# Kernel optimization log

Measured on AMD Instinct MI355X. Metric: run time of the kernel, lower is better.

Reference implementation:

```python
import jax, jax.numpy as jnp
import numpy as np

B, T, D = 1, 1024, 1024
H = 16; HKV = 16; HD = D // H; R = 2; K = 3; LOWR = 32
HR = HKV * R                      # heads after harmonic expansion
OUTW = HKV * HD * 2 * R           # w_proj output width
SCALE = HD ** -0.5


def setup_inputs() -> dict:
    key = jax.random.key(0)
    ks = jax.random.split(key, 10)
    def rn(k, shape, sc=1.0):
        return jax.random.normal(k, shape, dtype=jnp.float32) * sc
    return {
        'hidden_states': rn(ks[0], (B, T, D)),
        'q_w': rn(ks[1], (D, D), D ** -0.5),
        'k_w': rn(ks[2], (D, D), D ** -0.5),
        'v_w': rn(ks[3], (D, D), D ** -0.5),
        'w1': rn(ks[4], (LOWR, D), D ** -0.5),
        'w2': rn(ks[5], (OUTW, LOWR), LOWR ** -0.5),
        'conv_w': rn(ks[6], (OUTW, K), K ** -0.5),
        'bt_w': rn(ks[7], (HKV * R, D), D ** -0.5),
        'bt_b': jnp.zeros((HKV * R,), jnp.float32),
        'o_w': rn(ks[8], (D, D * R), (D * R) ** -0.5),
        'omega': 0.01 * jnp.ones((1, 1, 1, R), jnp.float32),
        'phi': jnp.zeros((1, 1, 1, R), jnp.float32),
    }


def path_attention_forward(hidden_states, q_w, k_w, v_w, w1, w2, conv_w,
                           bt_w, bt_b, o_w, omega, phi):
    b, t, _ = hidden_states.shape
    q = hidden_states @ q_w.T
    k = hidden_states @ k_w.T
    v = hidden_states @ v_w.T
    # low-rank w projection, causal depthwise short conv (kernel K), SiLU
    w_raw = (hidden_states @ w1.T) @ w2.T                    # [b,t,OUTW]
    xp = jnp.pad(w_raw, ((0, 0), (K - 1, 0), (0, 0)))
    w_raw = sum(xp[:, i:i + t, :] * conv_w[:, i] for i in range(K))
    w_raw = jax.nn.silu(w_raw)
    # rotary-like harmonic mixing of Householder directions
    w5 = w_raw.reshape(b, t, HKV, 2 * R, HD)
    Ah = w5[:, :, :, 0::2, :]                                # [b,t,HKV,R,HD]
    Bh = w5[:, :, :, 1::2, :]
    pos = jnp.arange(t, dtype=jnp.float32)[None, :, None, None]
    theta = omega * pos + phi                                # [1,t,1,R]
    c = jnp.cos(theta)[..., None]
    s = jnp.sin(theta)[..., None]
    Wdir = Ah * c + Bh * s
    Wdir = Wdir * jax.lax.rsqrt(jnp.sum(Wdir * Wdir, -1, keepdims=True) + 1e-6)
    beta = jax.nn.sigmoid(hidden_states @ bt_w.T + bt_b) * 2.0   # [b,t,HR]
    # repeat-interleave q/k/v heads across harmonics -> [b,HR,t,HD]
    to_h = lambda x: jnp.swapaxes(jnp.repeat(x.reshape(b, t, H, HD), R, axis=2), 1, 2)
    qh, kh, vh = to_h(q), to_h(k), to_h(v)
    wh = jnp.swapaxes(Wdir.reshape(b, t, HR, HD), 1, 2)      # [b,HR,t,HD]
    bh = jnp.swapaxes(beta, 1, 2)                            # [b,HR,t]
    # PaTH logits: A_ij = q_i^T (H_i ... H_{j+1}) k_j, H_t = I - beta_t w_t w_t^T.
    # WY/UT transform: with M_ts = beta_t (w_t.w_s) for s<t, the coefficients
    # B_tj (t>j) of the accumulated rank-1 corrections solve the unit-lower
    # triangular system (I + M) B = strilow(Db W K^T), and
    # A = tril(Q K^T - tril(Q W^T) B).
    idx = jnp.arange(t)
    strict = idx[:, None] > idx[None, :]
    incl = idx[:, None] >= idx[None, :]
    Mw = jnp.where(strict, jnp.einsum('bhtd,bhsd->bhts', wh, wh) * bh[..., None], 0.0)
    rhs = jnp.where(strict, jnp.einsum('bhtd,bhjd->bhtj', wh, kh) * bh[..., None], 0.0)
    Bmat = jax.scipy.linalg.solve_triangular(Mw + jnp.eye(t, dtype=Mw.dtype), rhs, lower=True)
    qk = jnp.einsum('bhid,bhjd->bhij', qh, kh)
    qw = jnp.where(incl, jnp.einsum('bhid,bhtd->bhit', qh, wh), 0.0)
    logits = (qk - jnp.einsum('bhit,bhtj->bhij', qw, Bmat)) * SCALE
    logits = jnp.where(incl, logits, -1e30)
    p = jax.nn.softmax(logits, axis=-1)
    o = jnp.einsum('bhij,bhjd->bhid', p, vh)                 # [b,HR,t,HD]
    o = jnp.swapaxes(o, 1, 2).reshape(b, t, HR * HD)         # [b,t,D*R]
    return o @ o_w.T


def reference(hidden_states, q_w, k_w, v_w, w1, w2, conv_w, bt_w, bt_b, o_w, omega, phi):
    return path_attention_forward(hidden_states, q_w, k_w, v_w, w1, w2, conv_w,
                                  bt_w, bt_b, o_w, omega, phi)
```

## Files before the change

### kernel.cpp

```cpp
#include <hip/hip_runtime.h>
#include <math.h>

#define TTD 1024
#define DDM 1024
#define HDIM 64
#define PSC2 0.18033688011112042f
#define LS 72

typedef __attribute__((ext_vector_type(8))) __bf16 bf16x8;
typedef __attribute__((ext_vector_type(4))) float f32x4;
#define MFMA16(a,b,c) __builtin_amdgcn_mfma_f32_16x16x32_bf16(a,b,c,0,0,0)

#define STR_(x) #x
#define WAITVM(N) asm volatile("s_waitcnt vmcnt(" STR_(N) ")" ::: "memory")
#define BAR() do { __builtin_amdgcn_s_barrier(); asm volatile("" ::: "memory"); } while (0)
#define LGKBAR() do { asm volatile("s_waitcnt lgkmcnt(0)" ::: "memory"); \
                      __builtin_amdgcn_s_barrier(); asm volatile("" ::: "memory"); } while (0)
#define FULLBAR() do { asm volatile("s_waitcnt vmcnt(0) lgkmcnt(0)" ::: "memory"); \
                       __builtin_amdgcn_s_barrier(); asm volatile("" ::: "memory"); } while (0)

__device__ __forceinline__ ushort f2b(float f) {
  unsigned u = __builtin_bit_cast(unsigned, f);
  return (ushort)((u + 0x7fffu + ((u >> 16) & 1u)) >> 16);
}
__device__ __forceinline__ float b2f(ushort u) {
  unsigned v = (unsigned)u << 16;
  return __builtin_bit_cast(float, v);
}

__device__ __forceinline__ void gload_lds16(const ushort* g, ushort* l) {
  __builtin_amdgcn_global_load_lds(
      (const __attribute__((address_space(1))) unsigned*)g,
      (__attribute__((address_space(3))) unsigned*)l, 16, 0, 0);
}

#define SWZ(row, cc) (((row) * 8 + ((cc) ^ ((row) & 7))) * 8)
#define SWZE(row, col) (SWZ(row, (col) >> 3) + ((col) & 7))
#define SWZ2(row, cc) (((row) * 8 + ((cc) ^ (((row) & 7) ^ ((row) >> 3)))) * 8)
#define SWZ2E(row, col) (SWZ2(row, (col) >> 3) + ((col) & 7))

__device__ __forceinline__ void stage_tile(const ushort* gb, long gs, ushort* tile,
                                           int w, int l) {
  int sub = l >> 3, cc = (l & 7) ^ sub;
  #pragma unroll
  for (int it = 0; it < 2; ++it) {
    int q = w * 2 + it;
    gload_lds16(gb + (long)(q * 8 + sub) * gs + cc * 8, &tile[(q * 64 + l) * 8]);
  }
}

__device__ __forceinline__ bf16x8 frag(const ushort* tile, int row, int cc) {
  return *(const bf16x8*)&tile[SWZ(row, cc)];
}
__device__ __forceinline__ bf16x8 frag2(const ushort* tile, int row, int cc) {
  return *(const bf16x8*)&tile[SWZ2(row, cc)];
}

#define XT_PERH   557056L
#define OFF_X     0L
#define OFF_PZ    35651584L
#define OFF_HSB   35651584L
#define OFF_QWW   37748736L
#define OFF_KWW   39845888L
#define OFF_VWW   41943040L
#define OFF_W2B   44040192L
#define OFF_WLOWB 44302336L
#define OFF_TB    98566144L
#define OFF_OALL  98566144L
#define OFF_YB    102760448L
#define OFF_OWB   106954752L
#define OFF_WHB   111149056L
#define OFF_QB    115343360L
#define OFF_KB    117440512L
#define OFF_VTB   119537664L
#define OFF_BETA  121634816L
#define OFF_BW64  121765888L

#define CVT_TOTAL 6488064L
struct CvtSegs {
  const float* src[8];
  ushort* dst[8];
  long cnt[8];
};
__global__ __launch_bounds__(256) void cvt_all_kernel(CvtSegs sg) {
  long e = ((long)blockIdx.x * 256 + threadIdx.x) * 4;
  #pragma unroll
  for (int s = 0; s < 8; ++s) {
    if (e < sg.cnt[s]) {
      float4 f = *(const float4*)(sg.src[s] + e);
      ushort4 o;
      o.x = f2b(f.x); o.y = f2b(f.y); o.z = f2b(f.z); o.w = f2b(f.w);
      *(ushort4*)(sg.dst[s] + e) = o;
      return;
    }
    e -= sg.cnt[s];
  }
}

__global__ __launch_bounds__(256) void qkv_sp_kernel(
    const ushort* __restrict__ hsb,
    const ushort* __restrict__ wq, const ushort* __restrict__ wk, const ushort* __restrict__ wv,
    const ushort* __restrict__ bw, const float* __restrict__ bt_b,
    ushort* __restrict__ cq, ushort* __restrict__ ck, ushort* __restrict__ cv,
    float* __restrict__ beta, ushort* __restrict__ wlowb)
{
  int z = blockIdx.z;
  if (z == 3 && blockIdx.x != 0) return;
  const ushort* B = (z == 0) ? wq : (z == 1) ? wk : (z == 2) ? wv : bw;

  __shared__ ushort Ab[2][8192];
  __shared__ ushort Bb[2][4096];

  int tid = threadIdx.x, w = tid >> 6, l = tid & 63;
  int quad = l >> 4, lane15 = l & 15;
  int rm = blockIdx.y * 128, cn = (z == 3) ? 0 : blockIdx.x * 64;
  const ushort* Ag = hsb + (long)rm * DDM;
  const ushort* Bg = B + (long)cn * DDM;

  stage_tile(Ag, DDM, &Ab[0][0], w, l);
  stage_tile(Ag + 64 * DDM, DDM, &Ab[0][4096], w, l);
  stage_tile(Bg, DDM, &Bb[0][0], w, l);

  f32x4 acc[2][4] = {};
  int arow0 = (w & 1) * 32 + lane15;
  int asel = (w >> 1) * 4096;
  for (int kt = 0; kt < 16; ++kt) {
    int cur = kt & 1;
    if (kt < 15) {
      int nxt = cur ^ 1;
      stage_tile(Ag + (kt + 1) * 64, DDM, &Ab[nxt][0], w, l);
      stage_tile(Ag + 64 * DDM + (kt + 1) * 64, DDM, &Ab[nxt][4096], w, l);
      stage_tile(Bg + (kt + 1) * 64, DDM, &Bb[nxt][0], w, l);
      WAITVM(6);
    } else {
      WAITVM(0);
    }
    BAR();
    const ushort* Atile = &Ab[cur][asel];
    #pragma unroll
    for (int s = 0; s < 2; ++s) {
      bf16x8 a0 = frag(Atile, arow0, s * 4 + quad);
      bf16x8 a1 = frag(Atile, arow0 + 16, s * 4 + quad);
      #pragma unroll
      for (int f = 0; f < 4; ++f) {
        bf16x8 bf = frag(&Bb[cur][0], f * 16 + lane15, s * 4 + quad);
        acc[0][f] = MFMA16(a0, bf, acc[0][f]);
        acc[1][f] = MFMA16(a1, bf, acc[1][f]);
      }
    }
    BAR();
  }

  if (z < 2) {
    ushort* Cb = (z == 0) ? cq : ck;
    #pragma unroll
    for (int rr = 0; rr < 2; ++rr) {
      int orow = rm + w * 32 + rr * 16 + quad * 4;
      #pragma unroll
      for (int f = 0; f < 4; ++f)
        #pragma unroll
        for (int r = 0; r < 4; ++r)
          Cb[(long)(orow + r) * DDM + cn + f * 16 + lane15] = f2b(acc[rr][f][r]);
    }
  } else if (z == 2) {
    #pragma unroll
    for (int rr = 0; rr < 2; ++rr) {
      int orow = rm + w * 32 + rr * 16 + quad * 4;
      #pragma unroll
      for (int f = 0; f < 4; ++f) {
        ushort4 o;
        o.x = f2b(acc[rr][f][0]); o.y = f2b(acc[rr][f][1]);
        o.z = f2b(acc[rr][f][2]); o.w = f2b(acc[rr][f][3]);
        *(ushort4*)&cv[(long)(cn + f * 16 + lane15) * TTD + orow] = o;
      }
    }
  } else {
    #pragma unroll
    for (int rr = 0; rr < 2; ++rr) {
      int orow = rm + w * 32 + rr * 16 + quad * 4;
      #pragma unroll
      for (int f = 0; f < 2; ++f) {
        int hr = f * 16 + lane15;
        float bb = bt_b[hr];
        #pragma unroll
        for (int r = 0; r < 4; ++r)
          beta[(long)hr * TTD + orow + r] = 2.f / (1.f + __expf(-(acc[rr][f][r] + bb)));
      }
      #pragma unroll
      for (int f = 2; f < 4; ++f)
        #pragma unroll
        for (int r = 0; r < 4; ++r)
          wlowb[(long)(orow + r) * 32 + (f - 2) * 16 + lane15] = f2b(acc[rr][f][r]);
    }
  }
}

__global__ __launch_bounds__(256) void wraw_solveA_kernel(
    const ushort* __restrict__ wlowb, const ushort* __restrict__ w2b,
    const float* __restrict__ conv_w, const float* __restrict__ omega,
    const float* __restrict__ phi, const float* __restrict__ beta,
    ushort* __restrict__ whb, ushort* __restrict__ TB, ushort* __restrict__ YB)
{
  int c = blockIdx.x;
  int rm = c * 64;
  int p = blockIdx.y;
  int hkv = p >> 1, r = p & 1;
  int c0 = hkv * 256 + r * 128;

  __shared__ char pool_[65568];
  ushort* As = (ushort*)pool_;
  ushort* Bs = (ushort*)(pool_ + 4096);
  float (*WR)[132] = (float(*)[132])(pool_ + 12288);
  ushort* Wrow = (ushort*)(pool_ + 47136);
  ushort* WT   = (ushort*)(pool_ + 56352);
  float (*Lm)[65] = (float(*)[65])pool_;
  float (*Vf)[65] = (float(*)[65])(pool_ + 16640);
  ushort* Tb = (ushort*)(pool_ + 33280);

  int tid = threadIdx.x, w = tid >> 6, l = tid & 63;
  int quad = l >> 4, lane15 = l & 15;

  {
    int row = tid >> 2, ch = (tid & 3) * 8;
    gload_lds16(wlowb + (long)(rm + row) * 32 + ch, &As[row * 32 + ch]);
    gload_lds16(w2b + (long)(c0 + row) * 32 + ch, &Bs[row * 32 + ch]);
    gload_lds16(w2b + (long)(c0 + 64 + row) * 32 + ch, &Bs[(64 + row) * 32 + ch]);
  }
  {
    int hr2 = tid >> 7, col = tid & 127;
    float acc = 0.f;
    if (rm > 0) {
      long t = rm - 2 + hr2;
      for (int k = 0; k < 32; ++k)
        acc += b2f(wlowb[t * 32 + k]) * b2f(w2b[(long)(c0 + col) * 32 + k]);
    }
    WR[hr2][col] = acc;
  }
  FULLBAR();

  #pragma unroll
  for (int g = 0; g < 2; ++g) {
    f32x4 acc[4] = {};
    bf16x8 af = *(const bf16x8*)&As[(w * 16 + lane15) * 32 + quad * 8];
    #pragma unroll
    for (int f = 0; f < 4; ++f) {
      bf16x8 bf = *(const bf16x8*)&Bs[(g * 64 + f * 16 + lane15) * 32 + quad * 8];
      acc[f] = MFMA16(af, bf, acc[f]);
    }
    #pragma unroll
    for (int f = 0; f < 4; ++f)
      #pragma unroll
      for (int rr = 0; rr < 4; ++rr)
        WR[2 + w * 16 + quad * 4 + rr][g * 64 + f * 16 + lane15] = acc[f][rr];
  }
  LGKBAR();

  {
    float cwa[3], cwb[3];
    #pragma unroll
    for (int i = 0; i < 3; ++i) {
      cwa[i] = conv_w[(long)(c0 + l) * 3 + i];
      cwb[i] = conv_w[(long)(c0 + 64 + l) * 3 + i];
    }
    float om = omega[r], ph = phi[r];
    for (int it = 0; it < 16; ++it) {
      int tl = it * 4 + w;
      int t = rm + tl;
      float a = cwa[0] * WR[tl][l] + cwa[1] * WR[tl + 1][l] + cwa[2] * WR[tl + 2][l];
      float b = cwb[0] * WR[tl][64 + l] + cwb[1] * WR[tl + 1][64 + l] + cwb[2] * WR[tl + 2][64 + l];
      a = a / (1.f + __expf(-a));
      b = b / (1.f + __expf(-b));
      float th = om * (float)t + ph;
      float wd = a * __cosf(th) + b * __sinf(th);
      float ss = wd * wd;
      #pragma unroll
      for (int o = 32; o > 0; o >>= 1) ss += __shfl_xor(ss, o, 64);
      ushort hv = f2b(wd * (1.f / sqrtf(ss + 1e-6f)));
      whb[((long)p * TTD + t) * HDIM + l] = hv;
      Wrow[tl * LS + l] = hv;
      WT[l * LS + tl] = hv;
    }
  }
  LGKBAR();

  const float* bet = beta + (long)p * TTD + rm;
  ushort* TBh = TB + ((long)p * 16 + c) * 4096;
  ushort* YBh = YB + ((long)p * 16 + c) * 4096;

  f32x4 g4[4] = {};
  #pragma unroll
  for (int s = 0; s < 2; ++s) {
    bf16x8 af = *(const bf16x8*)&Wrow[(w * 16 + lane15) * LS + s * 32 + quad * 8];
    #pragma unroll
    for (int f = 0; f < 4; ++f) {
      bf16x8 bf = *(const bf16x8*)&Wrow[(f * 16 + lane15) * LS + s * 32 + quad * 8];
      g4[f] = MFMA16(af, bf, g4[f]);
    }
  }
  #pragma unroll
  for (int r4 = 0; r4 < 4; ++r4) {
    int t = w * 16 + quad * 4 + r4;
    float bv = bet[t];
    #pragma unroll
    for (int f = 0; f < 4; ++f) {
      int tp = f * 16 + lane15;
      Lm[t][tp] = (t > tp) ? bv * g4[f][r4] : 0.f;
    }
  }
  LGKBAR();

  {
    float cur[16];
    #pragma unroll
    for (int i = 0; i < 16; ++i) cur[i] = (w * 16 + i == l) ? bet[l] : 0.f;
    for (int sb = 0; sb < 4; ++sb) {
      if (w == sb) {
        float xloc[16];
        #pragma unroll
        for (int i = 0; i < 16; ++i) {
          float bv = cur[i];
          #pragma unroll
          for (int j2 = 0; j2 < 16; ++j2)
            if (j2 < i) bv -= Lm[sb * 16 + i][sb * 16 + j2] * xloc[j2];
          xloc[i] = bv;
          Vf[sb * 16 + i][l] = bv;
        }
      }
      LGKBAR();
      if (w > sb) {
        float xp[16];
        #pragma unroll
        for (int t = 0; t < 16; ++t) xp[t] = Vf[sb * 16 + t][l];
        #pragma unroll
        for (int i = 0; i < 16; ++i) {
          float s2 = cur[i];
          #pragma unroll
          for (int t = 0; t < 16; ++t) s2 -= Lm[w * 16 + i][sb * 16 + t] * xp[t];
          cur[i] = s2;
        }
      }
    }
  }
  {
    int t = tid >> 2, off = (tid & 3) * 16;
    ushort tmp[16];
    #pragma unroll
    for (int i = 0; i < 16; ++i) { tmp[i] = f2b(Vf[t][off + i]); Tb[t * LS + off + i] = tmp[i]; }
    *(uint4*)&TBh[t * 64 + off] = *(const uint4*)&tmp[0];
    *(uint4*)&TBh[t * 64 + off + 8] = *(const uint4*)&tmp[8];
  }
  LGKBAR();
  f32x4 y[4] = {};
  #pragma unroll
  for (int s = 0; s < 2; ++s) {
    bf16x8 af = *(const bf16x8*)&Tb[(w * 16 + lane15) * LS + s * 32 + quad * 8];
    #pragma unroll
    for (int f = 0; f < 4; ++f) {
      bf16x8 bf = *(const bf16x8*)&WT[(f * 16 + lane15) * LS + s * 32 + quad * 8];
      y[f] = MFMA16(af, bf, y[f]);
    }
  }
  #pragma unroll
  for (int f = 0; f < 4; ++f)
    #pragma unroll
    for (int r4 = 0; r4 < 4; ++r4)
      YBh[(long)(w * 16 + quad * 4 + r4) * 64 + f * 16 + lane15] = f2b(y[f][r4]);
}

__global__ __launch_bounds__(256) void solveB_kernel(
    const ushort* __restrict__ whb, const ushort* __restrict__ kb,
    const ushort* __restrict__ TB, const ushort* __restrict__ YB,
    ushort* __restrict__ Xb, ushort* __restrict__ KZ)
{
  int h = blockIdx.x;
  int ty = blockIdx.y;
  int js = (ty < 8) ? ty : (23 - ty);
  int j0 = js * 64;
  const ushort* wh_h = whb + (long)h * TTD * HDIM;
  const ushort* k_h = kb + (long)(h >> 1) * 64;
  ushort* X_h = Xb + (long)h * XT_PERH;
  ushort* KZ_h = KZ + (long)h * 15 * TTD * HDIM;
  int xidx = js * 16 - js * (js - 1) / 2;

  __shared__ ushort KT[4096];
  __shared__ ushort WT[4096];
  __shared__ ushort XM[4096];
  __shared__ ushort nS[4096];

  int tid = threadIdx.x, w = tid >> 6, l = tid & 63;
  int quad = l >> 4, lane15 = l & 15;
  f32x4 Sacc[4] = {}, Wacc[4] = {};

  stage_tile(k_h + (long)j0 * DDM, DDM, KT, w, l);

  float kreg[4][4];
  #pragma unroll
  for (int f = 0; f < 4; ++f)
    #pragma unroll
    for (int r = 0; r < 4; ++r)
      kreg[f][r] = b2f(k_h[(long)(j0 + w * 16 + quad * 4 + r) * DDM + f * 16 + lane15]);

  int prow0 = tid >> 3, pd0 = (tid & 7) * 8;
  uint4 pk0 = *(const uint4*)&wh_h[((long)js * 64 + prow0) * HDIM + pd0];
  uint4 pk1 = *(const uint4*)&wh_h[((long)js * 64 + 32 + prow0) * HDIM + pd0];
  bf16x8 ybr0 = {}, ybr1 = {};

  WAITVM(0);

  for (int c = js; c < 16; ++c) {
    LGKBAR();
    {
      const ushort* pu0 = (const ushort*)&pk0;
      const ushort* pu1 = (const ushort*)&pk1;
      #pragma unroll
      for (int i = 0; i < 8; ++i) WT[SWZ2E(pd0 + i, prow0)] = pu0[i];
      #pragma unroll
      for (int i = 0; i < 8; ++i) WT[SWZ2E(pd0 + i, 32 + prow0)] = pu1[i];
    }
    if (c < 15) {
      pk0 = *(const uint4*)&wh_h[((long)(c + 1) * 64 + prow0) * HDIM + pd0];
      pk1 = *(const uint4*)&wh_h[((long)(c + 1) * 64 + 32 + prow0) * HDIM + pd0];
    }
    f32x4 xacc[4] = {};
    if (c == js) {
      const ushort* whc = wh_h + (long)c * 64 * HDIM;
      f32x4 m[4] = {};
      #pragma unroll
      for (int s = 0; s < 2; ++s) {
        bf16x8 af = *(const bf16x8*)&whc[(long)(w * 16 + lane15) * HDIM + s * 32 + quad * 8];
        #pragma unroll
        for (int f = 0; f < 4; ++f)
          m[f] = MFMA16(af, frag(KT, f * 16 + lane15, s * 4 + quad), m[f]);
      }
      #pragma unroll
      for (int f = 0; f < 4; ++f)
        #pragma unroll
        for (int r = 0; r < 4; ++r) {
          int t = w * 16 + quad * 4 + r, j = f * 16 + lane15;
          XM[SWZE(j, t)] = (t > j) ? f2b(m[f][r]) : (ushort)0;
        }
      LGKBAR();
      const ushort* TBh = TB + ((long)h * 16 + c) * 4096;
      #pragma unroll
      for (int s = 0; s < 2; ++s) {
        bf16x8 af = *(const bf16x8*)&TBh[(long)(w * 16 + lane15) * 64 + s * 32 + quad * 8];
        #pragma unroll
        for (int f = 0; f < 4; ++f)
          xacc[f] = MFMA16(af, frag(XM, f * 16 + lane15, s * 4 + quad), xacc[f]);
      }
      LGKBAR();
    } else {
      #pragma unroll
      for (int f = 0; f < 4; ++f) {
        xacc[f] = MFMA16(ybr0, frag(KT, f * 16 + lane15, 0 * 4 + quad), xacc[f]);
        xacc[f] = MFMA16(ybr0, frag(nS, f * 16 + lane15, 0 * 4 + quad), xacc[f]);
        xacc[f] = MFMA16(ybr1, frag(KT, f * 16 + lane15, 1 * 4 + quad), xacc[f]);
        xacc[f] = MFMA16(ybr1, frag(nS, f * 16 + lane15, 1 * 4 + quad), xacc[f]);
      }
    }
    #pragma unroll
    for (int f = 0; f < 4; ++f)
      #pragma unroll
      for (int r = 0; r < 4; ++r)
        XM[SWZE(f * 16 + lane15, w * 16 + quad * 4 + r)] = f2b(xacc[f][r]);
    LGKBAR();
    {
      ushort* xt = X_h + (long)xidx * 4096;
      int j = tid >> 2, c2 = (tid & 3) * 2;
      bf16x8 s0 = frag(XM, j, c2);
      bf16x8 s1 = frag(XM, j, c2 + 1);
      *(bf16x8*)&xt[j * 64 + c2 * 8] = s0;
      *(bf16x8*)&xt[j * 64 + c2 * 8 + 8] = s1;
    }
    ++xidx;
    if (c < 15) {
      {
        const ushort* YBn = YB + ((long)h * 16 + c + 1) * 4096;
        ybr0 = *(const bf16x8*)&YBn[(long)(w * 16 + lane15) * 64 + 0 * 32 + quad * 8];
        ybr1 = *(const bf16x8*)&YBn[(long)(w * 16 + lane15) * 64 + 1 * 32 + quad * 8];
      }
      #pragma unroll
      for (int s = 0; s < 2; ++s) {
        bf16x8 aw = frag2(WT, w * 16 + lane15, s * 4 + quad);
        bf16x8 ax = frag(XM, w * 16 + lane15, s * 4 + quad);
        #pragma unroll
        for (int f = 0; f < 4; ++f) {
          Sacc[f] = MFMA16(aw, frag(XM, f * 16 + lane15, s * 4 + quad), Sacc[f]);
          Wacc[f] = MFMA16(ax, frag2(WT, f * 16 + lane15, s * 4 + quad), Wacc[f]);
        }
      }
      ushort* pz = KZ_h + (long)c * TTD * HDIM;
      #pragma unroll
      for (int f = 0; f < 4; ++f)
        #pragma unroll
        for (int r = 0; r < 4; ++r)
          pz[(long)(j0 + w * 16 + quad * 4 + r) * 64 + f * 16 + lane15] =
              f2b(kreg[f][r] - Wacc[f][r]);
      #pragma unroll
      for (int f = 0; f < 4; ++f)
        #pragma unroll
        for (int r = 0; r < 4; ++r)
          nS[SWZE(f * 16 + lane15, w * 16 + quad * 4 + r)] = f2b(-Sacc[f][r]);
    }
  }
}

__global__ __launch_bounds__(256) void flash_kernel(
    const ushort* __restrict__ qb, const ushort* __restrict__ kbuf,
    const ushort* __restrict__ whb, const ushort* __restrict__ Xb,
    const ushort* __restrict__ KZ, const ushort* __restrict__ vTb,
    ushort* __restrict__ oall)
{
  int h = blockIdx.x;
  int y = blockIdx.y;
  int ri = (y < 8) ? y : (23 - y);
  int r0 = ri * 64;
  const ushort* q_h = qb + (long)(h >> 1) * 64;
  const ushort* k_h = kbuf + (long)(h >> 1) * 64;
  const ushort* wh_h = whb + (long)h * TTD * HDIM;
  const ushort* X_h = Xb + (long)h * XT_PERH;
  const ushort* kz = KZ + ((long)h * 15 + (ri - 1)) * TTD * HDIM;
  const ushort* v_h = vTb + (long)(h >> 1) * 64 * TTD;

  __shared__ ushort S[2][3][4096];
  __shared__ ushort KD[4096];
  __shared__ ushort QWD[4096];
  __shared__ ushort PT[4096];

  int tid = threadIdx.x, w = tid >> 6, l = tid & 63;
  int quad = l >> 4, lane15 = l & 15;

  bf16x8 aq[2];
  #pragma unroll
  for (int s = 0; s < 2; ++s)
    aq[s] = *(const bf16x8*)&q_h[(long)(r0 + w * 16 + lane15) * DDM + s * 32 + quad * 8];
  bf16x8 kones;
  #pragma unroll
  for (int i = 0; i < 8; ++i) kones[i] = (__bf16)1.0f;
  const ushort* xst = X_h + (long)ri * 4096;
  stage_tile(k_h + (long)r0 * DDM, DDM, KD, w, l);
  if (ri > 0) stage_tile(kz, 64, &S[0][0][0], w, l);
  stage_tile(xst, 64, &S[0][1][0], w, l);
  stage_tile(v_h, TTD, &S[0][2][0], w, l);
  {
    f32x4 t4[4] = {};
    #pragma unroll
    for (int s = 0; s < 2; ++s)
      #pragma unroll
      for (int f = 0; f < 4; ++f) {
        bf16x8 bf = *(const bf16x8*)&wh_h[(long)(r0 + f * 16 + lane15) * HDIM + s * 32 + quad * 8];
        t4[f] = MFMA16(aq[s], bf, t4[f]);
      }
    #pragma unroll
    for (int f = 0; f < 4; ++f)
      #pragma unroll
      for (int r = 0; r < 4; ++r) {
        int i = w * 16 + quad * 4 + r, t = f * 16 + lane15;
        QWD[SWZE(i, t)] = (i >= t) ? f2b(-t4[f][r]) : (ushort)0;
      }
  }

  f32x4 O[4] = {};
  f32x4 O5 = {};
  float m[4];
  #pragma unroll
  for (int r = 0; r < 4; ++r) m[r] = -1e30f;

  for (int jb = 0; jb <= ri; ++jb) {
    int cur = jb & 1;
    const ushort* xnx = xst + (long)(15 - jb) * 4096;
    if (jb < ri) {
      long c0n = (long)(jb + 1) * 64;
      ushort* nb = &S[cur ^ 1][0][0];
      if (jb + 1 < ri) {
        stage_tile(kz + c0n * 64, 64, nb, w, l);
        stage_tile(xnx, 64, nb + 4096, w, l);
        stage_tile(v_h + c0n, TTD, nb + 8192, w, l);
        WAITVM(6);
      } else {
        stage_tile(xnx, 64, nb + 4096, w, l);
        stage_tile(v_h + c0n, TTD, nb + 8192, w, l);
        WAITVM(4);
      }
    } else {
      WAITVM(0);
    }
    BAR();
    const ushort* Skz = &S[cur][0][0];
    const ushort* Sx  = &S[cur][1][0];
    const ushort* Sv  = &S[cur][2][0];
    f32x4 acc[4] = {};
    const ushort* Sb = (jb < ri) ? Skz : KD;
    #pragma unroll
    for (int s = 0; s < 2; ++s)
      #pragma unroll
      for (int f = 0; f < 4; ++f)
        acc[f] = MFMA16(aq[s], frag(Sb, f * 16 + lane15, s * 4 + quad), acc[f]);
    #pragma unroll
    for (int s = 0; s < 2; ++s) {
      bf16x8 aw = frag(QWD, w * 16 + lane15, s * 4 + quad);
      #pragma unroll
      for (int f = 0; f < 4; ++f)
        acc[f] = MFMA16(aw, frag(Sx, f * 16 + lane15, s * 4 + quad), acc[f]);
    }
    float rmax[4] = {-3e38f, -3e38f, -3e38f, -3e38f};
    #pragma unroll
    for (int f = 0; f < 4; ++f)
      #pragma unroll
      for (int r = 0; r < 4; ++r) {
        float lv = acc[f][r] * PSC2;
        if (jb == ri && (f * 16 + lane15) > (w * 16 + quad * 4 + r)) lv = -3e38f;
        acc[f][r] = lv;
        rmax[r] = fmaxf(rmax[r], lv);
      }
    #pragma unroll
    for (int r = 0; r < 4; ++r) {
      rmax[r] = fmaxf(rmax[r], __shfl_xor(rmax[r], 1, 64));
      rmax[r] = fmaxf(rmax[r], __shfl_xor(rmax[r], 2, 64));
      rmax[r] = fmaxf(rmax[r], __shfl_xor(rmax[r], 4, 64));
      rmax[r] = fmaxf(rmax[r], __shfl_xor(rmax[r], 8, 64));
    }
    bool grow = (rmax[0] > m[0]) | (rmax[1] > m[1]) | (rmax[2] > m[2]) | (rmax[3] > m[3]);
    if (__any(grow)) {
      float alpha[4];
      #pragma unroll
      for (int r = 0; r < 4; ++r) {
        float nm = fmaxf(m[r], rmax[r]);
        alpha[r] = exp2f(m[r] - nm);
        m[r] = nm;
        O5[r] *= alpha[r];
      }
      #pragma unroll
      for (int f = 0; f < 4; ++f)
        #pragma unroll
        for (int r = 0; r < 4; ++r) O[f][r] *= alpha[r];
    }
    #pragma unroll
    for (int f = 0; f < 4; ++f)
      #pragma unroll
      for (int r = 0; r < 4; ++r)
        acc[f][r] = exp2f(acc[f][r] - m[r]);
    #pragma unroll
    for (int f = 0; f < 4; ++f)
      #pragma unroll
      for (int r = 0; r < 4; ++r) {
        int i = w * 16 + quad * 4 + r;
        PT[SWZE(i, f * 16 + lane15)] = f2b(acc[f][r]);
      }
    #pragma unroll
    for (int s = 0; s < 2; ++s) {
      bf16x8 ap = frag(PT, w * 16 + lane15, s * 4 + quad);
      #pragma unroll
      for (int f = 0; f < 4; ++f)
        O[f] = MFMA16(ap, frag(Sv, f * 16 + lane15, s * 4 + quad), O[f]);
      O5 = MFMA16(ap, kones, O5);
    }
    BAR();
    xst = xnx;
  }
  float lsum[4];
  #pragma unroll
  for (int r = 0; r < 4; ++r) lsum[r] = 1.f / O5[r];
  #pragma unroll
  for (int f = 0; f < 4; ++f)
    #pragma unroll
    for (int r = 0; r < 4; ++r)
      oall[(long)(r0 + w * 16 + quad * 4 + r) * 2048 + h * 64 + f * 16 + lane15] =
          f2b(O[f][r] * lsum[r]);
}

__global__ __launch_bounds__(256) void gemm_out_kernel(
    const ushort* __restrict__ A, const ushort* __restrict__ Bb, float* __restrict__ C)
{
  __shared__ ushort Ab[2][8192];
  __shared__ ushort Bt[2][8192];
  int tid = threadIdx.x, w = tid >> 6, l = tid & 63;
  int quad = l >> 4, lane15 = l & 15;
  int rm = blockIdx.y * 64, cn = blockIdx.x * 64;
  const ushort* Ag = A + (long)rm * 2048;
  const ushort* Bg = Bb + (long)cn * 2048;

  stage_tile(Ag, 2048, &Ab[0][0], w, l);
  stage_tile(Ag + 64, 2048, &Ab[0][4096], w, l);
  stage_tile(Bg, 2048, &Bt[0][0], w, l);
  stage_tile(Bg + 64, 2048, &Bt[0][4096], w, l);

  f32x4 acc[4] = {};
  for (int kt = 0; kt < 16; ++kt) {
    int cur = kt & 1;
    if (kt < 15) {
      int nxt = cur ^ 1;
      long o = (long)(kt + 1) * 128;
      stage_tile(Ag + o, 2048, &Ab[nxt][0], w, l);
      stage_tile(Ag + o + 64, 2048, &Ab[nxt][4096], w, l);
      stage_tile(Bg + o, 2048, &Bt[nxt][0], w, l);
      stage_tile(Bg + o + 64, 2048, &Bt[nxt][4096], w, l);
      WAITVM(8);
    } else {
      WAITVM(0);
    }
    BAR();
    #pragma unroll
    for (int u = 0; u < 2; ++u)
      #pragma unroll
      for (int s = 0; s < 2; ++s) {
        bf16x8 af = frag(&Ab[cur][u * 4096], w * 16 + lane15, s * 4 + quad);
        #pragma unroll
        for (int f = 0; f < 4; ++f)
          acc[f] = MFMA16(af, frag(&Bt[cur][u * 4096], f * 16 + lane15, s * 4 + quad), acc[f]);
      }
    BAR();
  }
  int orow = rm + w * 16 + quad * 4;
  #pragma unroll
  for (int f = 0; f < 4; ++f)
    #pragma unroll
    for (int r = 0; r < 4; ++r)
      C[(long)(orow + r) * DDM + cn + f * 16 + lane15] = acc[f][r];
}

extern "C" void kernel_launch(void* const* d_in, const int* in_sizes, int n_in,
                              void* d_out, int out_size, void* d_ws, size_t ws_size,
                              hipStream_t stream) {
  const float* hs     = (const float*)d_in[0];
  const float* q_w    = (const float*)d_in[1];
  const float* k_w    = (const float*)d_in[2];
  const float* v_w    = (const float*)d_in[3];
  const float* w1     = (const float*)d_in[4];
  const float* w2     = (const float*)d_in[5];
  const float* conv_w = (const float*)d_in[6];
  const float* bt_w   = (const float*)d_in[7];
  const float* bt_b   = (const float*)d_in[8];
  const float* o_w    = (const float*)d_in[9];
  const float* omega  = (const float*)d_in[10];
  const float* phi    = (const float*)d_in[11];
  float* out = (float*)d_out;
  char* ws = (char*)d_ws;

  ushort* Xb     = (ushort*)(ws + OFF_X);
  ushort* KZb    = (ushort*)(ws + OFF_PZ);
  ushort* hs_b   = (ushort*)(ws + OFF_HSB);
  ushort* qw_wb  = (ushort*)(ws + OFF_QWW);
  ushort* kw_wb  = (ushort*)(ws + OFF_KWW);
  ushort* vw_wb  = (ushort*)(ws + OFF_VWW);
  ushort* w2_b   = (ushort*)(ws + OFF_W2B);
  ushort* wlow_b = (ushort*)(ws + OFF_WLOWB);
  ushort* TB     = (ushort*)(ws + OFF_TB);
  ushort* o_all  = (ushort*)(ws + OFF_OALL);
  ushort* YB     = (ushort*)(ws + OFF_YB);
  ushort* ow_b   = (ushort*)(ws + OFF_OWB);
  ushort* wh_b   = (ushort*)(ws + OFF_WHB);
  ushort* q_b    = (ushort*)(ws + OFF_QB);
  ushort* k_b    = (ushort*)(ws + OFF_KB);
  ushort* vT_b   = (ushort*)(ws + OFF_VTB);
  float*  beta   = (float*)(ws + OFF_BETA);
  ushort* bw_b   = (ushort*)(ws + OFF_BW64);

  CvtSegs sg;
  sg.src[0] = hs;   sg.dst[0] = hs_b;          sg.cnt[0] = 1048576;
  sg.src[1] = q_w;  sg.dst[1] = qw_wb;         sg.cnt[1] = 1048576;
  sg.src[2] = k_w;  sg.dst[2] = kw_wb;         sg.cnt[2] = 1048576;
  sg.src[3] = v_w;  sg.dst[3] = vw_wb;         sg.cnt[3] = 1048576;
  sg.src[4] = w2;   sg.dst[4] = w2_b;          sg.cnt[4] = 131072;
  sg.src[5] = bt_w; sg.dst[5] = bw_b;          sg.cnt[5] = 32768;
  sg.src[6] = w1;   sg.dst[6] = bw_b + 32768;  sg.cnt[6] = 32768;
  sg.src[7] = o_w;  sg.dst[7] = ow_b;          sg.cnt[7] = 2097152;
  cvt_all_kernel<<<dim3((CVT_TOTAL + 1023) / 1024), 256, 0, stream>>>(sg);

  qkv_sp_kernel<<<dim3(16, 8, 4), 256, 0, stream>>>(
      hs_b, qw_wb, kw_wb, vw_wb, bw_b, bt_b, q_b, k_b, vT_b, beta, wlow_b);

  wraw_solveA_kernel<<<dim3(16, 32), 256, 0, stream>>>(
      wlow_b, w2_b, conv_w, omega, phi, beta, wh_b, TB, YB);

  solveB_kernel<<<dim3(32, 16), 256, 0, stream>>>(wh_b, k_b, TB, YB, Xb, KZb);

  flash_kernel<<<dim3(32, 16), 256, 0, stream>>>(q_b, k_b, wh_b, Xb, KZb, vT_b, o_all);

  gemm_out_kernel<<<dim3(16, 16), 256, 0, stream>>>(o_all, ow_b, out);

  (void)in_sizes; (void)n_in; (void)out_size; (void)ws_size;
}
```

Before: 207.5 us.

## Split flash attention key range across two blocks and merge partials

```diff
diff --git a/kernel.cpp b/kernel.cpp
--- a/kernel.cpp
+++ b/kernel.cpp
@@ -75,6 +75,8 @@
 #define OFF_VTB   119537664L
 #define OFF_BETA  121634816L
 #define OFF_BW64  121765888L
+#define OFF_PO    121896960L
+#define OFF_PML   138674176L
 
 #define CVT_TOTAL 6488064L
 struct CvtSegs {
@@ -509,11 +511,15 @@
     const ushort* __restrict__ qb, const ushort* __restrict__ kbuf,
     const ushort* __restrict__ whb, const ushort* __restrict__ Xb,
     const ushort* __restrict__ KZ, const ushort* __restrict__ vTb,
-    ushort* __restrict__ oall)
+    float* __restrict__ partO, float* __restrict__ partML)
 {
   int h = blockIdx.x;
   int y = blockIdx.y;
-  int ri = (y < 8) ? y : (23 - y);
+  int ri = 15 - (y >> 1);
+  int half = y & 1;
+  int nlo = (ri + 1) >> 1;
+  int jb0 = half ? nlo : 0;
+  int jb1 = half ? ri : (nlo - 1);
   int r0 = ri * 64;
   const ushort* q_h = qb + (long)(h >> 1) * 64;
   const ushort* k_h = kbuf + (long)(h >> 1) * 64;
@@ -523,7 +529,6 @@
   const ushort* v_h = vTb + (long)(h >> 1) * 64 * TTD;
 
   __shared__ ushort S[2][3][4096];
-  __shared__ ushort KD[4096];
   __shared__ ushort QWD[4096];
   __shared__ ushort PT[4096];
 
@@ -537,11 +542,15 @@
   bf16x8 kones;
   #pragma unroll
   for (int i = 0; i < 8; ++i) kones[i] = (__bf16)1.0f;
-  const ushort* xst = X_h + (long)ri * 4096;
-  stage_tile(k_h + (long)r0 * DDM, DDM, KD, w, l);
-  if (ri > 0) stage_tile(kz, 64, &S[0][0][0], w, l);
-  stage_tile(xst, 64, &S[0][1][0], w, l);
-  stage_tile(v_h, TTD, &S[0][2][0], w, l);
+
+  long xidx0 = (long)jb0 * 16 - (long)jb0 * (jb0 - 1) / 2 + (ri - jb0);
+  const ushort* xst = X_h + xidx0 * 4096;
+  if (jb0 <= jb1) {
+    if (jb0 == ri) stage_tile(k_h + (long)r0 * DDM, DDM, &S[0][0][0], w, l);
+    else           stage_tile(kz + (long)jb0 * 4096, 64, &S[0][0][0], w, l);
+    stage_tile(xst, 64, &S[0][1][0], w, l);
+    stage_tile(v_h + jb0 * 64, TTD, &S[0][2][0], w, l);
+  }
   {
     f32x4 t4[4] = {};
     #pragma unroll
@@ -566,31 +575,25 @@
   #pragma unroll
   for (int r = 0; r < 4; ++r) m[r] = -1e30f;
 
-  for (int jb = 0; jb <= ri; ++jb) {
-    int cur = jb & 1;
+  for (int jb = jb0; jb <= jb1; ++jb) {
+    int cur = (jb - jb0) & 1;
     const ushort* xnx = xst + (long)(15 - jb) * 4096;
-    if (jb < ri) {
-      long c0n = (long)(jb + 1) * 64;
+    if (jb < jb1) {
+      int jn = jb + 1;
       ushort* nb = &S[cur ^ 1][0][0];
-      if (jb + 1 < ri) {
-        stage_tile(kz + c0n * 64, 64, nb, w, l);
-        stage_tile(xnx, 64, nb + 4096, w, l);
-        stage_tile(v_h + c0n, TTD, nb + 8192, w, l);
-        WAITVM(6);
-      } else {
-        stage_tile(xnx, 64, nb + 4096, w, l);
-        stage_tile(v_h + c0n, TTD, nb + 8192, w, l);
-        WAITVM(4);
-      }
+      if (jn < ri) stage_tile(kz + (long)jn * 4096, 64, nb, w, l);
+      else         stage_tile(k_h + (long)r0 * DDM, DDM, nb, w, l);
+      stage_tile(xnx, 64, nb + 4096, w, l);
+      stage_tile(v_h + jn * 64, TTD, nb + 8192, w, l);
+      WAITVM(6);
     } else {
       WAITVM(0);
     }
     BAR();
-    const ushort* Skz = &S[cur][0][0];
-    const ushort* Sx  = &S[cur][1][0];
-    const ushort* Sv  = &S[cur][2][0];
+    const ushort* Sb = &S[cur][0][0];
+    const ushort* Sx = &S[cur][1][0];
+    const ushort* Sv = &S[cur][2][0];
     f32x4 acc[4] = {};
-    const ushort* Sb = (jb < ri) ? Skz : KD;
     #pragma unroll
     for (int s = 0; s < 2; ++s)
       #pragma unroll
@@ -658,15 +661,52 @@
     BAR();
     xst = xnx;
   }
-  float lsum[4];
-  #pragma unroll
-  for (int r = 0; r < 4; ++r) lsum[r] = 1.f / O5[r];
+  long p = ((long)h * 16 + ri) * 2 + half;
+  float* PO = partO + p * 4096;
+  float* PM = partML + p * 128;
   #pragma unroll
   for (int f = 0; f < 4; ++f)
     #pragma unroll
     for (int r = 0; r < 4; ++r)
-      oall[(long)(r0 + w * 16 + quad * 4 + r) * 2048 + h * 64 + f * 16 + lane15] =
-          f2b(O[f][r] * lsum[r]);
+      PO[(w * 16 + quad * 4 + r) * 64 + f * 16 + lane15] = O[f][r];
+  if (lane15 == 0) {
+    #pragma unroll
+    for (int r = 0; r < 4; ++r) {
+      int i = w * 16 + quad * 4 + r;
+      PM[i] = m[r];
+      PM[64 + i] = O5[r];
+    }
+  }
+}
+
+__global__ __launch_bounds__(256) void merge_kernel(
+    const float* __restrict__ PO, const float* __restrict__ PML,
+    ushort* __restrict__ oall)
+{
+  int h = blockIdx.x, ri = blockIdx.y;
+  int r0 = ri * 64;
+  long p0 = ((long)h * 16 + ri) * 2;
+  int tid = threadIdx.x;
+  int row = tid >> 2, c0 = (tid & 3) * 16;
+  float m1 = PML[p0 * 128 + row],      l1 = PML[p0 * 128 + 64 + row];
+  float m2 = PML[(p0 + 1) * 128 + row], l2 = PML[(p0 + 1) * 128 + 64 + row];
+  float M = fmaxf(m1, m2);
+  float a1 = exp2f(m1 - M), a2 = exp2f(m2 - M);
+  float inv = 1.f / (l1 * a1 + l2 * a2);
+  const float* O1 = PO + p0 * 4096 + row * 64 + c0;
+  const float* O2 = PO + (p0 + 1) * 4096 + row * 64 + c0;
+  ushort* dst = oall + (long)(r0 + row) * 2048 + h * 64 + c0;
+  #pragma unroll
+  for (int j4 = 0; j4 < 4; ++j4) {
+    float4 o1 = *(const float4*)(O1 + j4 * 4);
+    float4 o2 = *(const float4*)(O2 + j4 * 4);
+    ushort4 o;
+    o.x = f2b((o1.x * a1 + o2.x * a2) * inv);
+    o.y = f2b((o1.y * a1 + o2.y * a2) * inv);
+    o.z = f2b((o1.z * a1 + o2.z * a2) * inv);
+    o.w = f2b((o1.w * a1 + o2.w * a2) * inv);
+    *(ushort4*)(dst + j4 * 4) = o;
+  }
 }
 
 __global__ __launch_bounds__(256) void gemm_out_kernel(
@@ -755,6 +795,8 @@
   ushort* vT_b   = (ushort*)(ws + OFF_VTB);
   float*  beta   = (float*)(ws + OFF_BETA);
   ushort* bw_b   = (ushort*)(ws + OFF_BW64);
+  float*  partO  = (float*)(ws + OFF_PO);
+  float*  partML = (float*)(ws + OFF_PML);
 
   CvtSegs sg;
   sg.src[0] = hs;   sg.dst[0] = hs_b;          sg.cnt[0] = 1048576;
@@ -775,7 +817,9 @@
 
   solveB_kernel<<<dim3(32, 16), 256, 0, stream>>>(wh_b, k_b, TB, YB, Xb, KZb);
 
-  flash_kernel<<<dim3(32, 16), 256, 0, stream>>>(q_b, k_b, wh_b, Xb, KZb, vT_b, o_all);
+  flash_kernel<<<dim3(32, 32), 256, 0, stream>>>(
+      q_b, k_b, wh_b, Xb, KZb, vT_b, partO, partML);
+  merge_kernel<<<dim3(32, 16), 256, 0, stream>>>(partO, partML, o_all);
 
   gemm_out_kernel<<<dim3(16, 16), 256, 0, stream>>>(o_all, ow_b, out);
 
```

After: 208.7 us. No clear change (+0.5%).
